# Kernel tuning notes

Measured on AMD Instinct MI355X. Metric: run time of the kernel, lower is better.

Reference implementation:

```python
import jax, jax.numpy as jnp
import numpy as np
import math

D_MODEL = 512
N_HEADS = 8
D_K = D_MODEL // N_HEADS
B, S, KC = 16, 1024, 32
NEG = -1e32


def setup_inputs() -> dict:
    key = jax.random.key(0)
    ks = jax.random.split(key, 14)
    s = 1.0 / math.sqrt(D_MODEL)
    return {
        "q": jax.random.normal(ks[0], (B, S, D_MODEL), jnp.float32),
        "k": jax.random.normal(ks[1], (B, S, D_MODEL), jnp.float32),
        "v": jax.random.normal(ks[2], (B, S, D_MODEL), jnp.float32),
        "q_seq": jax.random.randint(ks[3], (B, S), 0, 500, jnp.int32),
        "c_seq": jax.random.randint(ks[4], (B, S, KC), 0, 2, jnp.int32),
        "Wq": jax.random.normal(ks[5], (D_MODEL, D_MODEL), jnp.float32) * s,
        "bq": jnp.zeros((D_MODEL,), jnp.float32),
        "Wk": jax.random.normal(ks[6], (D_MODEL, D_MODEL), jnp.float32) * s,
        "bk": jnp.zeros((D_MODEL,), jnp.float32),
        "Wv": jax.random.normal(ks[7], (D_MODEL, D_MODEL), jnp.float32) * s,
        "bv": jnp.zeros((D_MODEL,), jnp.float32),
        "Wo": jax.random.normal(ks[8], (D_MODEL, D_MODEL), jnp.float32) * s,
        "bo": jnp.zeros((D_MODEL,), jnp.float32),
    }


def qc_mask(q_seq, c_seq):
    # maskq[b,i,j] = 1 if same question id
    maskq = (q_seq[:, :, None] == q_seq[:, None, :]).astype(jnp.int32)
    # maskc[b,i,j] = 1 if any shared concept; entries are {0,1} so AND-sum == dot
    overlap = jnp.einsum("bik,bjk->bij", c_seq, c_seq)  # int32
    maskc = (overlap > 0).astype(jnp.int32)
    # strict lower triangle: 1 - triu(ones, k=0)
    tri = jnp.tril(jnp.ones((S, S), jnp.int32), k=-1)[None]
    return (maskc + maskq + 1) * tri  # values in {0,1,2,3}


def reference(q, k, v, q_seq, c_seq, Wq, bq, Wk, bk, Wv, bv, Wo, bo):
    bs = q.shape[0]
    # NOTE: original code swaps the linears: k<-k_linear(k), q<-v_linear(q), v<-q_linear(v)
    kh = (k @ Wk.T + bk).reshape(bs, S, N_HEADS, D_K).transpose(0, 2, 1, 3)
    qh = (q @ Wv.T + bv).reshape(bs, S, N_HEADS, D_K).transpose(0, 2, 1, 3)
    vh = (v @ Wq.T + bq).reshape(bs, S, N_HEADS, D_K).transpose(0, 2, 1, 3)

    mask = qc_mask(q_seq, c_seq)  # [B,S,S] int
    scores = jnp.einsum("bhid,bhjd->bhij", qh, kh) / math.sqrt(D_K)
    m = mask[:, None]  # [B,1,S,S]
    scores = jnp.where(m == 0, NEG, scores)
    scores = jax.nn.softmax(scores, axis=-1)

    adjustments = jnp.array([0.0, 0.5, 1.0, 2.0], jnp.float32)
    adjusted = scores * adjustments[m]
    sums = jnp.sum(scores, axis=-1, keepdims=True)
    sums = jnp.where(sums == 0, jnp.ones_like(sums), sums)
    adjusted = adjusted / sums

    out = jnp.einsum("bhij,bhjd->bhid", adjusted, vh)
    concat = out.transpose(0, 2, 1, 3).reshape(bs, S, D_MODEL)
    return concat @ Wo.T + bo
```

## Files before the change

### kernel.cpp

```cpp
#include <hip/hip_runtime.h>
#include <stdint.h>

typedef unsigned short u16;
typedef unsigned int   u32;
typedef unsigned long long u64;
typedef __attribute__((ext_vector_type(8)))  short short8;
typedef __attribute__((ext_vector_type(4)))  float f32x4;
typedef __attribute__((ext_vector_type(16))) float f32x16;
typedef __attribute__((ext_vector_type(4)))  unsigned int u32x4;

__device__ __forceinline__ u16 f2bf(float f) {
  u32 u = __builtin_bit_cast(u32, f);
  u32 r = u + 0x7FFFu + ((u >> 16) & 1u);
  return (u16)(r >> 16);
}

__device__ __forceinline__ u32 cvtpk(float a, float b) {
  u32 r;
  asm("v_cvt_pk_bf16_f32 %0, %1, %2" : "=v"(r) : "v"(a), "v"(b));
  return r;
}

__device__ __forceinline__ void gload_lds16(const void* g, void* l) {
  __builtin_amdgcn_global_load_lds(
      (__attribute__((address_space(1))) void*)(uintptr_t)g,
      (__attribute__((address_space(3))) void*)(u32)(uintptr_t)l,
      16, 0, 0);
}

#define SB() __builtin_amdgcn_sched_barrier(0)

__global__ void cast4_kernel(const float* __restrict__ s0, const float* __restrict__ s1,
                             const float* __restrict__ s2, const float* __restrict__ s3,
                             u16* __restrict__ d0, u16* __restrict__ d1,
                             u16* __restrict__ d2, u16* __restrict__ d3, int n8) {
  const int sel = blockIdx.y;
  const float* src = sel == 0 ? s0 : sel == 1 ? s1 : sel == 2 ? s2 : s3;
  u16* dst = sel == 0 ? d0 : sel == 1 ? d1 : sel == 2 ? d2 : d3;
  int i = blockIdx.x * blockDim.x + threadIdx.x;
  if (i >= n8) return;
  const float4* s4 = (const float4*)src;
  float4 x = s4[2 * (size_t)i];
  float4 y = s4[2 * (size_t)i + 1];
  u32x4 r;
  r.x = cvtpk(x.x, x.y); r.y = cvtpk(x.z, x.w);
  r.z = cvtpk(y.x, y.y); r.w = cvtpk(y.z, y.w);
  *(u32x4*)(dst + 8 * (size_t)i) = r;
}

__global__ void pack_kernel(const int* __restrict__ q_seq, const int* __restrict__ c_seq,
                            int2* __restrict__ meta, int n) {
  int i = blockIdx.x * blockDim.x + threadIdx.x;
  if (i >= n) return;
  u32 bits = 0;
#pragma unroll
  for (int j = 0; j < 32; ++j)
    bits |= (c_seq[(size_t)i * 32 + j] != 0) ? (1u << j) : 0u;
  meta[i] = make_int2(q_seq[i], (int)bits);
}

__global__ __launch_bounds__(256) void mask_kernel(const int2* __restrict__ meta,
                                                   u64* __restrict__ maskw) {
  const int qc = blockIdx.x, kt = blockIdx.y, b = blockIdx.z;
  const int t = threadIdx.x;
  const int q = qc * 256 + t;
  __shared__ int2 colm[32];
  if (t < 32) colm[t] = meta[b * 1024 + kt * 32 + t];
  __syncthreads();
  const int2 qm = meta[b * 1024 + q];
  const int rs = qm.x; const u32 rb = (u32)qm.y;
  u64 w = 0;
#pragma unroll
  for (int j = 0; j < 32; ++j) {
    const int2 cm = colm[j];
    const int kj = kt * 32 + j;
    u32 m = 0;
    if (kj < q) m = 1u + (rs == cm.x ? 1u : 0u) + (((rb & (u32)cm.y) != 0u) ? 1u : 0u);
    w |= (u64)m << (2 * j);
  }
  maskw[((size_t)b * 32 + kt) * 1024 + q] = w;
}

__global__ __launch_bounds__(256) void gemm_qkv(const float* __restrict__ qf,
                                                const float* __restrict__ kf,
                                                const float* __restrict__ vf,
                                                const u16* __restrict__ Wcat,
                                                const float* __restrict__ bv,
                                                const float* __restrict__ bk,
                                                const float* __restrict__ bq,
                                                u16* __restrict__ qhb,
                                                u16* __restrict__ khb,
                                                u16* __restrict__ vTb,
                                                float kscale) {
  const int K = 512;
  __shared__ __align__(16) u16 As[128 * 64];
  __shared__ __align__(16) u16 Bs[128 * 64];
  const int t    = threadIdx.x;
  const int lane = t & 63;
  const int wid  = t >> 6;
  const int g    = lane >> 4, l15 = lane & 15;
  const int wm   = wid >> 1, wn = wid & 1;
  const int wrk  = (blockIdx.x & 7) * 192 + (blockIdx.x >> 3);
  const int mb   = wrk >> 2, nbi = wrk & 3;
  const int which = mb >> 7;
  const float* Ax = which == 0 ? qf : which == 1 ? kf : vf;
  const float* bias = which == 0 ? bv : which == 1 ? bk : bq;
  const float scale = which == 1 ? kscale : 1.0f;
  u16* outb = which == 0 ? qhb : which == 1 ? khb : vTb;
  const int mloc = (mb & 127) << 7;
  const int n0   = nbi << 7;
  const u16* W   = Wcat + (size_t)which * 512 * 512;

  const int srow = t >> 3;
  const int scol = (((t & 7) ^ (srow & 7)) << 3);
  const int dcol = ((t & 7) << 3);
  const int rsw  = l15 & 7;

  f32x4 acc[4][4];
#pragma unroll
  for (int i = 0; i < 4; ++i)
#pragma unroll
    for (int j = 0; j < 4; ++j) acc[i][j] = f32x4{0.f, 0.f, 0.f, 0.f};

  float4 ax[4], ay[4];
#pragma unroll
  for (int i = 0; i < 4; ++i) {
    const float* src = Ax + (size_t)(mloc + 32 * i + srow) * K + scol;
    ax[i] = *(const float4*)src;
    ay[i] = *(const float4*)(src + 4);
  }

  for (int k0 = 0; k0 < K; k0 += 64) {
    SB();
    __builtin_amdgcn_s_barrier();
    SB();
#pragma unroll
    for (int i = 0; i < 4; ++i)
      gload_lds16(W + (size_t)(n0 + i * 32 + srow) * K + k0 + scol,
                  Bs + i * 2048 + t * 8);
#pragma unroll
    for (int i = 0; i < 4; ++i) {
      u32x4 r;
      r.x = cvtpk(ax[i].x, ax[i].y); r.y = cvtpk(ax[i].z, ax[i].w);
      r.z = cvtpk(ay[i].x, ay[i].y); r.w = cvtpk(ay[i].z, ay[i].w);
      *(u32x4*)(As + (32 * i + srow) * 64 + dcol) = r;
    }
    SB();
    const int kn = (k0 + 64) & (K - 1);
#pragma unroll
    for (int i = 0; i < 4; ++i) {
      const float* src = Ax + (size_t)(mloc + 32 * i + srow) * K + kn + scol;
      ax[i] = *(const float4*)src;
      ay[i] = *(const float4*)(src + 4);
    }
    SB();
    asm volatile("s_waitcnt vmcnt(8) lgkmcnt(0)" ::: "memory");
    __builtin_amdgcn_s_barrier();
    SB();
#pragma unroll
    for (int kk = 0; kk < 2; ++kk) {
      short8 a[4], b[4];
#pragma unroll
      for (int mi = 0; mi < 4; ++mi)
        a[mi] = *(const short8*)(As + (wm * 64 + mi * 16 + l15) * 64
                                 + (((kk * 4 + g) ^ rsw) << 3));
#pragma unroll
      for (int ni = 0; ni < 4; ++ni)
        b[ni] = *(const short8*)(Bs + (wn * 64 + ni * 16 + l15) * 64
                                 + (((kk * 4 + g) ^ rsw) << 3));
#pragma unroll
      for (int mi = 0; mi < 4; ++mi)
#pragma unroll
        for (int ni = 0; ni < 4; ++ni)
          acc[mi][ni] = __builtin_amdgcn_mfma_f32_16x16x32_bf16(a[mi], b[ni], acc[mi][ni], 0, 0, 0);
    }
  }
  asm volatile("s_waitcnt vmcnt(0)" ::: "memory");

#pragma unroll
  for (int ni = 0; ni < 4; ++ni) {
    const int col = n0 + wn * 64 + ni * 16 + l15;
    const float bz = bias[col];
#pragma unroll
    for (int mi = 0; mi < 4; ++mi) {
#pragma unroll
      for (int r = 0; r < 4; ++r) {
        const int row = mloc + wm * 64 + mi * 16 + g * 4 + r;
        const u16 val = f2bf((acc[mi][ni][r] + bz) * scale);
        const size_t base = ((size_t)(row >> 10) * 8 + (col >> 6)) * 65536;
        const int s = row & 1023, d = col & 63;
        if (which == 0) {
          outb[base + (size_t)s * 64 + d] = val;
        } else if (which == 1) {
          outb[base + (s >> 5) * 2048 + (d >> 3) * 256 + (s & 31) * 8 + (d & 7)] = val;
        } else {
          outb[base + (s >> 3) * 512 + d * 8 + (s & 7)] = val;
        }
      }
    }
  }
}

__global__ __launch_bounds__(256) void gemm_out(const u16* __restrict__ A,
                                                const u16* __restrict__ W,
                                                const float* __restrict__ bias,
                                                float* __restrict__ outp) {
  const int K = 512, N = 512;
  __shared__ __align__(16) u16 As[128 * 64];
  __shared__ __align__(16) u16 Bs[128 * 64];
  const int t    = threadIdx.x;
  const int lane = t & 63;
  const int wid  = t >> 6;
  const int g    = lane >> 4, l15 = lane & 15;
  const int wm   = wid >> 1, wn = wid & 1;
  const int wrk  = (blockIdx.x & 7) * 64 + (blockIdx.x >> 3);
  const int mb   = wrk >> 2, nbi = wrk & 3;
  const int m0   = mb << 7, n0 = nbi << 7;
  const int srow = t >> 3;
  const int scol = (((t & 7) ^ (srow & 7)) << 3);
  const int rsw  = l15 & 7;

  f32x4 acc[4][4];
#pragma unroll
  for (int i = 0; i < 4; ++i)
#pragma unroll
    for (int j = 0; j < 4; ++j) acc[i][j] = f32x4{0.f, 0.f, 0.f, 0.f};

  for (int k0 = 0; k0 < 512; k0 += 64) {
    SB();
    __builtin_amdgcn_s_barrier();
    SB();
#pragma unroll
    for (int i = 0; i < 4; ++i) {
      gload_lds16(A + (size_t)(m0 + i * 32 + srow) * K + k0 + scol, As + i * 2048 + t * 8);
      gload_lds16(W + (size_t)(n0 + i * 32 + srow) * K + k0 + scol, Bs + i * 2048 + t * 8);
    }
    SB();
    asm volatile("s_waitcnt vmcnt(0)" ::: "memory");
    __builtin_amdgcn_s_barrier();
    SB();
#pragma unroll
    for (int kk = 0; kk < 2; ++kk) {
      short8 a[4], b[4];
#pragma unroll
      for (int mi = 0; mi < 4; ++mi)
        a[mi] = *(const short8*)(As + (wm * 64 + mi * 16 + l15) * 64
                                 + (((kk * 4 + g) ^ rsw) << 3));
#pragma unroll
      for (int ni = 0; ni < 4; ++ni)
        b[ni] = *(const short8*)(Bs + (wn * 64 + ni * 16 + l15) * 64
                                 + (((kk * 4 + g) ^ rsw) << 3));
#pragma unroll
      for (int mi = 0; mi < 4; ++mi)
#pragma unroll
        for (int ni = 0; ni < 4; ++ni)
          acc[mi][ni] = __builtin_amdgcn_mfma_f32_16x16x32_bf16(a[mi], b[ni], acc[mi][ni], 0, 0, 0);
    }
  }

#pragma unroll
  for (int ni = 0; ni < 4; ++ni) {
    const int col = n0 + wn * 64 + ni * 16 + l15;
    const float bz = bias[col];
#pragma unroll
    for (int mi = 0; mi < 4; ++mi)
#pragma unroll
      for (int r = 0; r < 4; ++r) {
        const int row = m0 + wm * 64 + mi * 16 + g * 4 + r;
        outp[(size_t)row * N + col] = acc[mi][ni][r] + bz;
      }
  }
}

__global__ __launch_bounds__(256, 4) void attn_kernel(const u16* __restrict__ qh,
                                                      const u16* __restrict__ kh,
                                                      const u16* __restrict__ vT,
                                                      const u64* __restrict__ maskw,
                                                      u16* __restrict__ outc) {
  const int h  = blockIdx.x;
  const int qp = blockIdx.y;
  const int b  = blockIdx.z;
  const int lane = threadIdx.x & 63;
  const int wid  = threadIdx.x >> 6;
  const int pair = wid >> 1, p = wid & 1;
  const int l31 = lane & 31;
  const int hh  = lane >> 5;
  const int hh8 = hh << 3, fourh = hh << 2, eighth = hh << 3;
  const int jt = pair ? (31 - qp) : qp;
  const int q0 = jt << 5;
  const int qi = q0 + l31;
  const size_t bh = (size_t)b * 8 + h;
  const u16* Q  = qh + bh * 65536;
  const u16* Kp = kh + bh * 65536;
  const u16* Vt = vT + bh * 65536;
  const u64* mrow = maskw + (size_t)b * 32768 + qi;

  __shared__ float mO[2][32][64];
  __shared__ float mL[2][64];
  __shared__ __align__(16) float Sl[2][32];

  short8 qB[4];
#pragma unroll
  for (int i = 0; i < 4; ++i)
    qB[i] = *(const short8*)(Q + (size_t)qi * 64 + i * 16 + eighth);

  f32x16 O0, O1;
#pragma unroll
  for (int i = 0; i < 16; ++i) { O0[i] = 0.f; O1[i] = 0.f; }
  float lr[4] = {0.f, 0.f, 0.f, 0.f};

  const int nt = jt + 1;

  short8 kA[4];
#pragma unroll
  for (int i = 0; i < 4; ++i)
    kA[i] = *(const short8*)(Kp + p * 2048 + ((2 * i + hh) * 32 + l31) * 8);
  u64 wm = mrow[(size_t)p << 10];

  for (int t = p; t < nt; t += 2) {
    const int k0 = t << 5;

    f32x16 S;
#pragma unroll
    for (int i = 0; i < 16; ++i) S[i] = 0.f;
#pragma unroll
    for (int i = 0; i < 4; ++i)
      S = __builtin_amdgcn_mfma_f32_32x32x16_bf16(kA[i], qB[i], S, 0, 0, 0);

    u64 wmn = 0;
    if (t + 2 < nt) {
#pragma unroll
      for (int i = 0; i < 4; ++i)
        kA[i] = *(const short8*)(Kp + (t + 2) * 2048 + ((2 * i + hh) * 32 + l31) * 8);
      wmn = mrow[(size_t)(t + 2) << 10];
    }

    short8 vB[2][2];
#pragma unroll
    for (int t4 = 0; t4 < 2; ++t4)
#pragma unroll
      for (int j = 0; j < 2; ++j)
        vB[t4][j] = *(const short8*)(Vt + (size_t)(t * 4 + t4 * 2 + hh) * 512 + (32 * j + l31) * 8);

    const u32 wsh0 = ((u32)wm) >> hh8;
    const u32 wsh1 = ((u32)(wm >> 32)) >> hh8;
    u32 pk[8];
#pragma unroll
    for (int s = 0; s < 4; ++s) {
      const u32 wsel = (s < 2) ? wsh0 : wsh1;
      float pv[4];
#pragma unroll
      for (int r = 0; r < 4; ++r) {
        const int m = 4 * s + r;
        const u32 m2 = (wsel >> (2 * r + 16 * (s & 1))) & 3u;
        float e;
        asm("v_exp_f32 %0, %1" : "=v"(e) : "v"(S[m]));
        const float pp = (m2 != 0u) ? e : 0.f;
        lr[r] += pp;
        asm("v_ldexp_f32 %0, %1, %2" : "=v"(pv[r]) : "v"(pp), "v"(m2));
      }
      pk[2 * s]     = cvtpk(pv[0], pv[1]);
      pk[2 * s + 1] = cvtpk(pv[2], pv[3]);
    }
    wm = wmn;

#pragma unroll
    for (int t4 = 0; t4 < 2; ++t4) {
      u32 a0 = pk[4 * t4 + 0], b0 = pk[4 * t4 + 2];
      u32 a1 = pk[4 * t4 + 1], b1 = pk[4 * t4 + 3];
      asm("v_permlane32_swap_b32 %0, %1" : "+v"(a0), "+v"(b0));
      asm("v_permlane32_swap_b32 %0, %1" : "+v"(a1), "+v"(b1));
      u32x4 w; w.x = a0; w.y = a1; w.z = b0; w.w = b1;
      const short8 pa = __builtin_bit_cast(short8, w);
      O0 = __builtin_amdgcn_mfma_f32_32x32x16_bf16(pa, vB[t4][0], O0, 0, 0, 0);
      O1 = __builtin_amdgcn_mfma_f32_32x32x16_bf16(pa, vB[t4][1], O1, 0, 0, 0);
    }
  }

  float lrun = (lr[0] + lr[1]) + (lr[2] + lr[3]);

  if (p == 1) {
#pragma unroll
    for (int r = 0; r < 16; ++r) {
      mO[pair][r][lane]      = O0[r];
      mO[pair][16 + r][lane] = O1[r];
    }
    mL[pair][lane] = lrun;
  }
  __syncthreads();
  if (p == 0) {
#pragma unroll
    for (int r = 0; r < 16; ++r) {
      O0[r] += mO[pair][r][lane];
      O1[r] += mO[pair][16 + r][lane];
    }
    lrun += mL[pair][lane];

    const float ssum = lrun + __shfl_xor(lrun, 32);
    if (lane < 32) Sl[pair][l31] = (ssum > 0.f) ? 0.25f / ssum : 0.f;
    __builtin_amdgcn_sched_barrier(0);
    asm volatile("s_waitcnt lgkmcnt(0)" ::: "memory");
    __builtin_amdgcn_sched_barrier(0);
#pragma unroll
    for (int t2 = 0; t2 < 4; ++t2) {
      const float4 inv4 = *(const float4*)&Sl[pair][8 * t2 + fourh];
#pragma unroll
      for (int r = 0; r < 4; ++r) {
        const int m = 4 * t2 + r;
        const float iv = (r == 0) ? inv4.x : (r == 1) ? inv4.y : (r == 2) ? inv4.z : inv4.w;
        const int qrow = q0 + 8 * t2 + fourh + r;
        u16* op = outc + ((size_t)b * 1024 + qrow) * 512 + h * 64;
        op[l31]      = f2bf(O0[m] * iv);
        op[32 + l31] = f2bf(O1[m] * iv);
      }
    }
  }
}

extern "C" void kernel_launch(void* const* d_in, const int* in_sizes, int n_in,
                              void* d_out, int out_size, void* d_ws, size_t ws_size,
                              hipStream_t stream) {
  (void)in_sizes; (void)n_in; (void)out_size; (void)ws_size;
  const float* q    = (const float*)d_in[0];
  const float* k    = (const float*)d_in[1];
  const float* v    = (const float*)d_in[2];
  const int*  q_seq = (const int*)d_in[3];
  const int*  c_seq = (const int*)d_in[4];
  const float* Wq   = (const float*)d_in[5];
  const float* bq   = (const float*)d_in[6];
  const float* Wk   = (const float*)d_in[7];
  const float* bk   = (const float*)d_in[8];
  const float* Wv   = (const float*)d_in[9];
  const float* bv   = (const float*)d_in[10];
  const float* Wo   = (const float*)d_in[11];
  const float* bo   = (const float*)d_in[12];
  float* out = (float*)d_out;

  char* ws = (char*)d_ws;
  const size_t SZH = 16ull * 8 * 1024 * 64 * 2;
  u16* qhb   = (u16*)(ws + 0 * SZH);
  u16* khb   = (u16*)(ws + 1 * SZH);
  u16* vTb   = (u16*)(ws + 2 * SZH);
  u16* attnc = (u16*)(ws + 3 * SZH);
  u16* Wvb = (u16*)(ws + 4 * SZH + 0 * 524288);
  u16* Wkb = (u16*)(ws + 4 * SZH + 1 * 524288);
  u16* Wqb = (u16*)(ws + 4 * SZH + 2 * 524288);
  u16* Wob = (u16*)(ws + 4 * SZH + 3 * 524288);
  int2* meta  = (int2*)(ws + 4 * SZH + 4 * 524288);
  u64* maskw  = (u64*)(ws + 4 * SZH + 4 * 524288 + 131072);

  const int n8w = 512 * 512 / 8;
  cast4_kernel<<<dim3(n8w / 256, 4), 256, 0, stream>>>(Wv, Wk, Wq, Wo,
                                                       Wvb, Wkb, Wqb, Wob, n8w);
  pack_kernel<<<64, 256, 0, stream>>>(q_seq, c_seq, meta, 16384);
  mask_kernel<<<dim3(4, 32, 16), 256, 0, stream>>>(meta, maskw);

  const float KSCALE = 0.18033688011112042f;
  gemm_qkv<<<dim3(1536), 256, 0, stream>>>(q, k, v, Wvb, bv, bk, bq,
                                           qhb, khb, vTb, KSCALE);
  attn_kernel<<<dim3(8, 16, 16), 256, 0, stream>>>(qhb, khb, vTb, maskw, attnc);
  gemm_out<<<512, 256, 0, stream>>>(attnc, Wob, bo, out);
}
```

Baseline: 144.8 us.

## Use 256x256 tiles with double-buffered LDS in QKV and output GEMMs

Both projection GEMMs move from 128x128 tiles with 256 threads to 256x256 tiles with 512 threads (8 waves, each computing 128x64), and add a two-stage LDS double buffer so the next k-tile loads while MFMAs run on the current one. The aim is higher arithmetic intensity per block and less barrier-exposed load latency. In exchange the grids shrink to 384 and 128 blocks, which may underfill the GPU's compute units, especially for gemm_out. Register pressure also rises with 32 accumulator tiles per thread, and LDS use grows to 128KB per block.

```diff
diff --git a/kernel.cpp b/kernel.cpp
--- a/kernel.cpp
+++ b/kernel.cpp
@@ -81,111 +81,130 @@
   maskw[((size_t)b * 32 + kt) * 1024 + q] = w;
 }
 
-__global__ __launch_bounds__(256) void gemm_qkv(const float* __restrict__ qf,
-                                                const float* __restrict__ kf,
-                                                const float* __restrict__ vf,
-                                                const u16* __restrict__ Wcat,
-                                                const float* __restrict__ bv,
-                                                const float* __restrict__ bk,
-                                                const float* __restrict__ bq,
-                                                u16* __restrict__ qhb,
-                                                u16* __restrict__ khb,
-                                                u16* __restrict__ vTb,
-                                                float kscale) {
+__global__ __launch_bounds__(512, 2) void gemm_qkv(const float* __restrict__ qf,
+                                                   const float* __restrict__ kf,
+                                                   const float* __restrict__ vf,
+                                                   const u16* __restrict__ Wcat,
+                                                   const float* __restrict__ bv,
+                                                   const float* __restrict__ bk,
+                                                   const float* __restrict__ bq,
+                                                   u16* __restrict__ qhb,
+                                                   u16* __restrict__ khb,
+                                                   u16* __restrict__ vTb,
+                                                   float kscale) {
   const int K = 512;
-  __shared__ __align__(16) u16 As[128 * 64];
-  __shared__ __align__(16) u16 Bs[128 * 64];
+  __shared__ __align__(16) u16 As[2][256 * 64];
+  __shared__ __align__(16) u16 Bs[2][256 * 64];
   const int t    = threadIdx.x;
   const int lane = t & 63;
-  const int wid  = t >> 6;
+  const int w    = t >> 6;
   const int g    = lane >> 4, l15 = lane & 15;
-  const int wm   = wid >> 1, wn = wid & 1;
-  const int wrk  = (blockIdx.x & 7) * 192 + (blockIdx.x >> 3);
-  const int mb   = wrk >> 2, nbi = wrk & 3;
-  const int which = mb >> 7;
-  const float* Ax = which == 0 ? qf : which == 1 ? kf : vf;
+  const int wm   = w >> 2, wn = w & 3;
+  const int wrk  = (blockIdx.x & 7) * 48 + (blockIdx.x >> 3);
+  const int mb   = wrk >> 1, nbi = wrk & 1;
+  const int which = mb >> 6;
+  const float* Ax   = which == 0 ? qf : which == 1 ? kf : vf;
   const float* bias = which == 0 ? bv : which == 1 ? bk : bq;
   const float scale = which == 1 ? kscale : 1.0f;
   u16* outb = which == 0 ? qhb : which == 1 ? khb : vTb;
-  const int mloc = (mb & 127) << 7;
-  const int n0   = nbi << 7;
+  const int mloc = (mb & 63) << 8;
+  const int n0   = nbi << 8;
   const u16* W   = Wcat + (size_t)which * 512 * 512;
 
   const int srow = t >> 3;
   const int scol = (((t & 7) ^ (srow & 7)) << 3);
-  const int dcol = ((t & 7) << 3);
   const int rsw  = l15 & 7;
 
-  f32x4 acc[4][4];
-#pragma unroll
-  for (int i = 0; i < 4; ++i)
+  f32x4 acc[8][4];
+#pragma unroll
+  for (int i = 0; i < 8; ++i)
 #pragma unroll
     for (int j = 0; j < 4; ++j) acc[i][j] = f32x4{0.f, 0.f, 0.f, 0.f};
 
   float4 ax[4], ay[4];
-#pragma unroll
-  for (int i = 0; i < 4; ++i) {
-    const float* src = Ax + (size_t)(mloc + 32 * i + srow) * K + scol;
-    ax[i] = *(const float4*)src;
-    ay[i] = *(const float4*)(src + 4);
-  }
-
-  for (int k0 = 0; k0 < K; k0 += 64) {
-    SB();
+
+#define LOAD_A(kt)                                                            \
+  {                                                                           \
+    _Pragma("unroll")                                                         \
+    for (int i = 0; i < 4; ++i) {                                             \
+      const float* src = Ax + (size_t)(mloc + 64 * i + srow) * K + (kt) * 64 + scol; \
+      ax[i] = *(const float4*)src;                                            \
+      ay[i] = *(const float4*)(src + 4);                                      \
+    }                                                                         \
+  }
+#define STAGE_B(kt, buf)                                                      \
+  {                                                                           \
+    _Pragma("unroll")                                                         \
+    for (int i = 0; i < 4; ++i)                                               \
+      gload_lds16(W + (size_t)(n0 + 64 * i + srow) * K + (kt) * 64 + scol,    \
+                  &Bs[buf][i * 4096 + t * 8]);                                \
+  }
+#define WRITE_A(buf)                                                          \
+  {                                                                           \
+    _Pragma("unroll")                                                         \
+    for (int i = 0; i < 4; ++i) {                                             \
+      u32x4 r;                                                                \
+      r.x = cvtpk(ax[i].x, ax[i].y); r.y = cvtpk(ax[i].z, ax[i].w);           \
+      r.z = cvtpk(ay[i].x, ay[i].y); r.w = cvtpk(ay[i].z, ay[i].w);           \
+      *(u32x4*)(&As[buf][i * 4096 + t * 8]) = r;                              \
+    }                                                                         \
+  }
+#define COMPUTE(buf)                                                          \
+  {                                                                           \
+    _Pragma("unroll")                                                         \
+    for (int kk = 0; kk < 2; ++kk) {                                          \
+      short8 a[8], b[4];                                                      \
+      _Pragma("unroll")                                                       \
+      for (int mi = 0; mi < 8; ++mi)                                          \
+        a[mi] = *(const short8*)(&As[buf][(wm * 128 + mi * 16 + l15) * 64     \
+                                 + (((kk * 4 + g) ^ rsw) << 3)]);             \
+      _Pragma("unroll")                                                       \
+      for (int ni = 0; ni < 4; ++ni)                                          \
+        b[ni] = *(const short8*)(&Bs[buf][(wn * 64 + ni * 16 + l15) * 64      \
+                                 + (((kk * 4 + g) ^ rsw) << 3)]);             \
+      _Pragma("unroll")                                                       \
+      for (int mi = 0; mi < 8; ++mi)                                          \
+        _Pragma("unroll")                                                     \
+        for (int ni = 0; ni < 4; ++ni)                                        \
+          acc[mi][ni] = __builtin_amdgcn_mfma_f32_16x16x32_bf16(a[mi], b[ni], acc[mi][ni], 0, 0, 0); \
+    }                                                                         \
+  }
+
+  LOAD_A(0); SB();
+  STAGE_B(0, 0); SB();
+  asm volatile("s_waitcnt vmcnt(4)" ::: "memory");
+  WRITE_A(0); SB();
+  asm volatile("s_waitcnt vmcnt(0) lgkmcnt(0)" ::: "memory");
+  __builtin_amdgcn_s_barrier();
+  SB();
+
+  for (int tt = 0; tt < 7; ++tt) {
+    const int cur = tt & 1, nxt = cur ^ 1;
+    LOAD_A(tt + 1); SB();
+    STAGE_B(tt + 1, nxt); SB();
+    COMPUTE(cur); SB();
+    asm volatile("s_waitcnt vmcnt(4)" ::: "memory");
+    WRITE_A(nxt); SB();
+    asm volatile("s_waitcnt vmcnt(0) lgkmcnt(0)" ::: "memory");
     __builtin_amdgcn_s_barrier();
     SB();
-#pragma unroll
-    for (int i = 0; i < 4; ++i)
-      gload_lds16(W + (size_t)(n0 + i * 32 + srow) * K + k0 + scol,
-                  Bs + i * 2048 + t * 8);
-#pragma unroll
-    for (int i = 0; i < 4; ++i) {
-      u32x4 r;
-      r.x = cvtpk(ax[i].x, ax[i].y); r.y = cvtpk(ax[i].z, ax[i].w);
-      r.z = cvtpk(ay[i].x, ay[i].y); r.w = cvtpk(ay[i].z, ay[i].w);
-      *(u32x4*)(As + (32 * i + srow) * 64 + dcol) = r;
-    }
-    SB();
-    const int kn = (k0 + 64) & (K - 1);
-#pragma unroll
-    for (int i = 0; i < 4; ++i) {
-      const float* src = Ax + (size_t)(mloc + 32 * i + srow) * K + kn + scol;
-      ax[i] = *(const float4*)src;
-      ay[i] = *(const float4*)(src + 4);
-    }
-    SB();
-    asm volatile("s_waitcnt vmcnt(8) lgkmcnt(0)" ::: "memory");
-    __builtin_amdgcn_s_barrier();
-    SB();
-#pragma unroll
-    for (int kk = 0; kk < 2; ++kk) {
-      short8 a[4], b[4];
-#pragma unroll
-      for (int mi = 0; mi < 4; ++mi)
-        a[mi] = *(const short8*)(As + (wm * 64 + mi * 16 + l15) * 64
-                                 + (((kk * 4 + g) ^ rsw) << 3));
-#pragma unroll
-      for (int ni = 0; ni < 4; ++ni)
-        b[ni] = *(const short8*)(Bs + (wn * 64 + ni * 16 + l15) * 64
-                                 + (((kk * 4 + g) ^ rsw) << 3));
-#pragma unroll
-      for (int mi = 0; mi < 4; ++mi)
-#pragma unroll
-        for (int ni = 0; ni < 4; ++ni)
-          acc[mi][ni] = __builtin_amdgcn_mfma_f32_16x16x32_bf16(a[mi], b[ni], acc[mi][ni], 0, 0, 0);
-    }
-  }
-  asm volatile("s_waitcnt vmcnt(0)" ::: "memory");
+  }
+  COMPUTE(1);
+
+#undef LOAD_A
+#undef STAGE_B
+#undef WRITE_A
+#undef COMPUTE
 
 #pragma unroll
   for (int ni = 0; ni < 4; ++ni) {
     const int col = n0 + wn * 64 + ni * 16 + l15;
     const float bz = bias[col];
 #pragma unroll
-    for (int mi = 0; mi < 4; ++mi) {
+    for (int mi = 0; mi < 8; ++mi) {
 #pragma unroll
       for (int r = 0; r < 4; ++r) {
-        const int row = mloc + wm * 64 + mi * 16 + g * 4 + r;
+        const int row = mloc + wm * 128 + mi * 16 + g * 4 + r;
         const u16 val = f2bf((acc[mi][ni][r] + bz) * scale);
         const size_t base = ((size_t)(row >> 10) * 8 + (col >> 6)) * 65536;
         const int s = row & 1023, d = col & 63;
@@ -201,72 +220,87 @@
   }
 }
 
-__global__ __launch_bounds__(256) void gemm_out(const u16* __restrict__ A,
-                                                const u16* __restrict__ W,
-                                                const float* __restrict__ bias,
-                                                float* __restrict__ outp) {
+__global__ __launch_bounds__(512, 2) void gemm_out(const u16* __restrict__ A,
+                                                   const u16* __restrict__ W,
+                                                   const float* __restrict__ bias,
+                                                   float* __restrict__ outp) {
   const int K = 512, N = 512;
-  __shared__ __align__(16) u16 As[128 * 64];
-  __shared__ __align__(16) u16 Bs[128 * 64];
+  __shared__ __align__(16) u16 As[2][256 * 64];
+  __shared__ __align__(16) u16 Bs[2][256 * 64];
   const int t    = threadIdx.x;
   const int lane = t & 63;
-  const int wid  = t >> 6;
+  const int w    = t >> 6;
   const int g    = lane >> 4, l15 = lane & 15;
-  const int wm   = wid >> 1, wn = wid & 1;
-  const int wrk  = (blockIdx.x & 7) * 64 + (blockIdx.x >> 3);
-  const int mb   = wrk >> 2, nbi = wrk & 3;
-  const int m0   = mb << 7, n0 = nbi << 7;
+  const int wm   = w >> 2, wn = w & 3;
+  const int wrk  = (blockIdx.x & 7) * 16 + (blockIdx.x >> 3);
+  const int mb   = wrk >> 1, nbi = wrk & 1;
+  const int m0   = mb << 8, n0 = nbi << 8;
   const int srow = t >> 3;
   const int scol = (((t & 7) ^ (srow & 7)) << 3);
   const int rsw  = l15 & 7;
 
-  f32x4 acc[4][4];
-#pragma unroll
-  for (int i = 0; i < 4; ++i)
+  f32x4 acc[8][4];
+#pragma unroll
+  for (int i = 0; i < 8; ++i)
 #pragma unroll
     for (int j = 0; j < 4; ++j) acc[i][j] = f32x4{0.f, 0.f, 0.f, 0.f};
 
-  for (int k0 = 0; k0 < 512; k0 += 64) {
-    SB();
-    __builtin_amdgcn_s_barrier();
-    SB();
-#pragma unroll
-    for (int i = 0; i < 4; ++i) {
-      gload_lds16(A + (size_t)(m0 + i * 32 + srow) * K + k0 + scol, As + i * 2048 + t * 8);
-      gload_lds16(W + (size_t)(n0 + i * 32 + srow) * K + k0 + scol, Bs + i * 2048 + t * 8);
-    }
-    SB();
+#define STAGE(kt, buf)                                                        \
+  {                                                                           \
+    _Pragma("unroll")                                                         \
+    for (int i = 0; i < 4; ++i) {                                             \
+      gload_lds16(A + (size_t)(m0 + 64 * i + srow) * K + (kt) * 64 + scol,    \
+                  &As[buf][i * 4096 + t * 8]);                                \
+      gload_lds16(W + (size_t)(n0 + 64 * i + srow) * K + (kt) * 64 + scol,    \
+                  &Bs[buf][i * 4096 + t * 8]);                                \
+    }                                                                         \
+  }
+#define COMPUTE(buf)                                                          \
+  {                                                                           \
+    _Pragma("unroll")                                                         \
+    for (int kk = 0; kk < 2; ++kk) {                                          \
+      short8 a[8], b[4];                                                      \
+      _Pragma("unroll")                                                       \
+      for (int mi = 0; mi < 8; ++mi)                                          \
+        a[mi] = *(const short8*)(&As[buf][(wm * 128 + mi * 16 + l15) * 64     \
+                                 + (((kk * 4 + g) ^ rsw) << 3)]);             \
+      _Pragma("unroll")                                                       \
+      for (int ni = 0; ni < 4; ++ni)                                          \
+        b[ni] = *(const short8*)(&Bs[buf][(wn * 64 + ni * 16 + l15) * 64      \
+                                 + (((kk * 4 + g) ^ rsw) << 3)]);             \
+      _Pragma("unroll")                                                       \
+      for (int mi = 0; mi < 8; ++mi)                                          \
+        _Pragma("unroll")                                                     \
+        for (int ni = 0; ni < 4; ++ni)                                        \
+          acc[mi][ni] = __builtin_amdgcn_mfma_f32_16x16x32_bf16(a[mi], b[ni], acc[mi][ni], 0, 0, 0); \
+    }                                                                         \
+  }
+
+  STAGE(0, 0); SB();
+  asm volatile("s_waitcnt vmcnt(0)" ::: "memory");
+  __builtin_amdgcn_s_barrier();
+  SB();
+  for (int tt = 0; tt < 7; ++tt) {
+    const int cur = tt & 1, nxt = cur ^ 1;
+    STAGE(tt + 1, nxt); SB();
+    COMPUTE(cur); SB();
     asm volatile("s_waitcnt vmcnt(0)" ::: "memory");
     __builtin_amdgcn_s_barrier();
     SB();
-#pragma unroll
-    for (int kk = 0; kk < 2; ++kk) {
-      short8 a[4], b[4];
-#pragma unroll
-      for (int mi = 0; mi < 4; ++mi)
-        a[mi] = *(const short8*)(As + (wm * 64 + mi * 16 + l15) * 64
-                                 + (((kk * 4 + g) ^ rsw) << 3));
-#pragma unroll
-      for (int ni = 0; ni < 4; ++ni)
-        b[ni] = *(const short8*)(Bs + (wn * 64 + ni * 16 + l15) * 64
-                                 + (((kk * 4 + g) ^ rsw) << 3));
-#pragma unroll
-      for (int mi = 0; mi < 4; ++mi)
-#pragma unroll
-        for (int ni = 0; ni < 4; ++ni)
-          acc[mi][ni] = __builtin_amdgcn_mfma_f32_16x16x32_bf16(a[mi], b[ni], acc[mi][ni], 0, 0, 0);
-    }
-  }
+  }
+  COMPUTE(1);
+#undef STAGE
+#undef COMPUTE
 
 #pragma unroll
   for (int ni = 0; ni < 4; ++ni) {
     const int col = n0 + wn * 64 + ni * 16 + l15;
     const float bz = bias[col];
 #pragma unroll
-    for (int mi = 0; mi < 4; ++mi)
+    for (int mi = 0; mi < 8; ++mi)
 #pragma unroll
       for (int r = 0; r < 4; ++r) {
-        const int row = m0 + wm * 64 + mi * 16 + g * 4 + r;
+        const int row = m0 + wm * 128 + mi * 16 + g * 4 + r;
         outp[(size_t)row * N + col] = acc[mi][ni][r] + bz;
       }
   }
@@ -456,8 +490,8 @@
   mask_kernel<<<dim3(4, 32, 16), 256, 0, stream>>>(meta, maskw);
 
   const float KSCALE = 0.18033688011112042f;
-  gemm_qkv<<<dim3(1536), 256, 0, stream>>>(q, k, v, Wvb, bv, bk, bq,
-                                           qhb, khb, vTb, KSCALE);
+  gemm_qkv<<<dim3(384), 512, 0, stream>>>(q, k, v, Wvb, bv, bk, bq,
+                                          qhb, khb, vTb, KSCALE);
   attn_kernel<<<dim3(8, 16, 16), 256, 0, stream>>>(qhb, khb, vTb, maskw, attnc);
-  gemm_out<<<512, 256, 0, stream>>>(attnc, Wob, bo, out);
-}
+  gemm_out<<<dim3(128), 512, 0, stream>>>(attnc, Wob, bo, out);
+}
```

Measured after the change: 155.2 us. +7.2%, slower.
